# Optimization experiments

Hardware: AMD Instinct MI355X
Metric: run time of the kernel (lower is better)

## Reference

```python
import jax, jax.numpy as jnp
import numpy as np

E, TOPK, H, F, CAP, TP = 8, 2, 1024, 4096, 2048, 1
N = 8192  # tokens * topk (token copies)


def setup_inputs() -> dict:
    key = jax.random.key(0)
    ks = jax.random.split(key, 6)
    inputs_shard = jax.random.normal(ks[0], (N, H), jnp.float32)
    gate_weight = jax.random.uniform(ks[1], (N,), jnp.float32)
    choosed_experts = jax.random.randint(ks[2], (N,), 0, E, dtype=jnp.int32)
    new_index = jax.random.permutation(ks[3], N).astype(jnp.int32)
    w1 = jax.random.normal(ks[4], (E, F, H), jnp.float32) * 0.02
    w2 = jax.random.normal(ks[5], (E, H, F), jnp.float32) * 0.02
    return {"inputs_shard": inputs_shard, "gate_weight": gate_weight,
            "choosed_experts": choosed_experts, "new_index": new_index,
            "w1": w1, "w2": w2}


def _grouped_expert_mlp(x, experts, w1, w2):
    # capacity-based grouped GEMM: sort token copies by expert, pack into
    # (E, CAP, H), run batched fc1->gelu->fc2, unpack back to token order.
    n = x.shape[0]
    order = jnp.argsort(experts)                      # [N]
    se = experts[order]
    offsets = jnp.searchsorted(se, jnp.arange(E))     # start of each expert block
    rank = jnp.arange(n) - offsets[se]                # within-expert position
    valid = rank < CAP                                # CAP=2*N/E, ~never drops
    slot = jnp.where(valid, se * CAP + rank, E * CAP) # out-of-range -> dropped
    buf = jnp.zeros((E * CAP, x.shape[1]), x.dtype).at[slot].set(x[order], mode="drop")
    xe = buf.reshape(E, CAP, -1)                      # [E, CAP, H]
    h = jax.nn.gelu(jnp.einsum("ech,efh->ecf", xe, w1), approximate=False)
    ye = jnp.einsum("ecf,ehf->ech", h, w2).reshape(E * CAP, -1)
    y_sorted = jnp.where(valid[:, None], ye[jnp.clip(slot, 0, E * CAP - 1)], 0.0)
    return jnp.zeros_like(x).at[order].set(y_sorted)  # back to token-copy order


def reference(inputs_shard, gate_weight, choosed_experts, new_index, w1, w2):
    # expert compute, scaled by router probabilities (combine-side scaling)
    result = _grouped_expert_mlp(inputs_shard, choosed_experts, w1, w2)
    result = result * gate_weight[:, None]
    # scatter combine: output1[new_index] = result; full_output += output1
    full_output = jnp.zeros((N, H), result.dtype).at[new_index].set(result)
    # topk reduce: view(N//topk, topk, H).sum(1)
    topk_reduce = full_output.reshape(N // TOPK, TOPK, H).sum(1)
    # reduce_scatter over TP group; TP=1 => identity
    return topk_reduce
```

## Files before the change

### kernel.cpp

```cpp
#include <hip/hip_runtime.h>
#include <stdint.h>

#define N_TOK 8192
#define HDIM  1024
#define FDIM  4096
#define NEXP  8
#define MAXTILES 72

typedef __attribute__((ext_vector_type(8))) __bf16 bf16x8;
typedef __attribute__((ext_vector_type(8))) unsigned short ushort8v;
typedef __attribute__((ext_vector_type(4))) unsigned short ushort4v;
typedef __attribute__((ext_vector_type(4))) float floatx4;

__device__ __forceinline__ unsigned short f2bf(float f) {
  union { float f; uint32_t u; } v; v.f = f;
  uint32_t u = v.u;
  return (unsigned short)((u + 0x7FFFu + ((u >> 16) & 1u)) >> 16);
}

__device__ __forceinline__ void load_lds16(const void* g, void* l) {
  __builtin_amdgcn_global_load_lds(
      (const __attribute__((address_space(1))) void*)(uintptr_t)g,
      (__attribute__((address_space(3))) void*)(uint32_t)(uintptr_t)l,
      16, 0, 0);
}


__global__ void k_count(const int* __restrict__ experts, int* __restrict__ meta) {
  int i = blockIdx.x * 256 + threadIdx.x;
  atomicAdd(&meta[experts[i]], 1);
}

__global__ void k_plan(int* __restrict__ meta) {
  if (threadIdx.x == 0) {
    int off = 0, nt = 0;
    for (int e = 0; e < NEXP; ++e) {
      int c = meta[e];
      meta[8 + e] = off;
      meta[16 + e] = off;
      int t = (c + 127) >> 7;
      for (int k = 0; k < t; ++k) meta[32 + nt++] = (e << 16) | k;
      off += c;
    }
    meta[24] = nt;
  }
}

__global__ void k_scatter(const int* __restrict__ experts, int* __restrict__ meta,
                          int* __restrict__ order) {
  int i = blockIdx.x * 256 + threadIdx.x;
  int e = experts[i];
  int pos = atomicAdd(&meta[16 + e], 1);
  order[pos] = i;
}

__global__ void k_pack(const float* __restrict__ x, const int* __restrict__ order,
                       unsigned short* __restrict__ xs) {
  int s = blockIdx.x;
  int i = order[s];
  int t = threadIdx.x;
  float4 v = *(const float4*)(x + (size_t)i * HDIM + t * 4);
  ushort4v u;
  u[0] = f2bf(v.x); u[1] = f2bf(v.y); u[2] = f2bf(v.z); u[3] = f2bf(v.w);
  *(ushort4v*)(xs + (size_t)s * HDIM + t * 4) = u;
}

__global__ void k_cvt(const float* __restrict__ src, unsigned short* __restrict__ dst) {
  size_t i = ((size_t)blockIdx.x * 256 + threadIdx.x) * 4;
  float4 v = *(const float4*)(src + i);
  ushort4v u;
  u[0] = f2bf(v.x); u[1] = f2bf(v.y); u[2] = f2bf(v.z); u[3] = f2bf(v.w);
  *(ushort4v*)(dst + i) = u;
}

template <bool PRE>
__global__ __launch_bounds__(256) void gemm1_t(
    const unsigned short* __restrict__ xs, const void* __restrict__ w1v,
    unsigned short* __restrict__ h1, const int* __restrict__ meta) {
  __shared__ unsigned short As[128 * 32];
  __shared__ unsigned short Bs[128 * 32];

  int bx = blockIdx.z;
  if (bx >= meta[24]) return;
  int entry = meta[32 + bx];
  int e = entry >> 16, mt = entry & 0xffff;
  int row0 = meta[8 + e] + mt * 128;
  int rend = meta[8 + e] + meta[e];
  int fBase = blockIdx.x * 128;

  int tid = threadIdx.x;
  int w = tid >> 6, lane = tid & 63;
  int r = lane & 15, q = lane >> 4;
  int wm = (w >> 1) * 64, wn = (w & 1) * 64;

  int ar0 = (w * 16) + (lane >> 2);
  int s0 = min(row0 + ar0, N_TOK - 1);
  int s1 = min(row0 + 64 + ar0, N_TOK - 1);
  const unsigned short* ag0 = xs + (size_t)s0 * HDIM + (lane & 3) * 8;
  const unsigned short* ag1 = xs + (size_t)s1 * HDIM + (lane & 3) * 8;
  unsigned short* al0 = &As[(w * 16) * 32];
  unsigned short* al1 = &As[(64 + w * 16) * 32];

  const unsigned short* bg0 = nullptr; const unsigned short* bg1 = nullptr;
  unsigned short* bl0 = nullptr; unsigned short* bl1 = nullptr;
  const float* wbase = nullptr; int brow = 0, bkk = 0;
  if constexpr (PRE) {
    const unsigned short* wb = (const unsigned short*)w1v;
    int br = w * 16 + (lane >> 2);
    bg0 = wb + ((size_t)e * FDIM + fBase + br) * HDIM + (lane & 3) * 8;
    bg1 = bg0 + (size_t)64 * HDIM;
    bl0 = &Bs[(w * 16) * 32];
    bl1 = &Bs[(64 + w * 16) * 32];
  } else {
    brow = tid >> 1; bkk = (tid & 1) * 16;
    wbase = (const float*)w1v + ((size_t)e * FDIM + fBase + brow) * HDIM + bkk;
  }

  floatx4 acc[4][4];
#pragma unroll
  for (int i = 0; i < 4; ++i)
#pragma unroll
    for (int j = 0; j < 4; ++j) acc[i][j] = (floatx4){0.f, 0.f, 0.f, 0.f};

  for (int k0 = 0; k0 < HDIM; k0 += 32) {
    __syncthreads();
    load_lds16(ag0 + k0, al0);
    load_lds16(ag1 + k0, al1);
    if constexpr (PRE) {
      load_lds16(bg0 + k0, bl0);
      load_lds16(bg1 + k0, bl1);
    } else {
      const float* gb = wbase + k0;
      float4 f0 = *(const float4*)(gb);
      float4 f1 = *(const float4*)(gb + 4);
      float4 f2 = *(const float4*)(gb + 8);
      float4 f3 = *(const float4*)(gb + 12);
      ushort8v u0, u1;
      u0[0] = f2bf(f0.x); u0[1] = f2bf(f0.y); u0[2] = f2bf(f0.z); u0[3] = f2bf(f0.w);
      u0[4] = f2bf(f1.x); u0[5] = f2bf(f1.y); u0[6] = f2bf(f1.z); u0[7] = f2bf(f1.w);
      u1[0] = f2bf(f2.x); u1[1] = f2bf(f2.y); u1[2] = f2bf(f2.z); u1[3] = f2bf(f2.w);
      u1[4] = f2bf(f3.x); u1[5] = f2bf(f3.y); u1[6] = f2bf(f3.z); u1[7] = f2bf(f3.w);
      *(ushort8v*)&Bs[brow * 32 + bkk] = u0;
      *(ushort8v*)&Bs[brow * 32 + bkk + 8] = u1;
    }
    __syncthreads();

    bf16x8 av[4], bv[4];
#pragma unroll
    for (int i = 0; i < 4; ++i)
      av[i] = __builtin_bit_cast(bf16x8, *(const ushort8v*)&As[(wm + i * 16 + r) * 32 + q * 8]);
#pragma unroll
    for (int j = 0; j < 4; ++j)
      bv[j] = __builtin_bit_cast(bf16x8, *(const ushort8v*)&Bs[(wn + j * 16 + r) * 32 + q * 8]);
#pragma unroll
    for (int i = 0; i < 4; ++i)
#pragma unroll
      for (int j = 0; j < 4; ++j)
        acc[i][j] = __builtin_amdgcn_mfma_f32_16x16x32_bf16(av[i], bv[j], acc[i][j], 0, 0, 0);
  }

#pragma unroll
  for (int i = 0; i < 4; ++i) {
    int mrow = row0 + wm + i * 16 + q * 4;
#pragma unroll
    for (int reg = 0; reg < 4; ++reg) {
      int s = mrow + reg;
      if (s < rend) {
        unsigned short* dst = h1 + (size_t)s * FDIM + fBase + wn + r;
#pragma unroll
        for (int j = 0; j < 4; ++j) {
          float v = acc[i][j][reg];
          float g = 0.5f * v * (1.0f + erff(v * 0.70710678118654752f));
          dst[j * 16] = f2bf(g);
        }
      }
    }
  }
}

template <bool PRE>
__global__ __launch_bounds__(256) void gemm2_t(
    const unsigned short* __restrict__ h1, const void* __restrict__ w2v,
    const float* __restrict__ gate, const int* __restrict__ new_index,
    float* __restrict__ out, const int* __restrict__ meta) {
  __shared__ unsigned short As[128 * 32];
  __shared__ unsigned short Bs[128 * 32];

  int bx = blockIdx.z;
  if (bx >= meta[24]) return;
  int entry = meta[32 + bx];
  int e = entry >> 16, mt = entry & 0xffff;
  int row0 = meta[8 + e] + mt * 128;
  int rend = meta[8 + e] + meta[e];
  int nBase = blockIdx.x * 128;
  int kStart = blockIdx.y * (FDIM / 2);
  int kEnd = kStart + (FDIM / 2);
  const int* order = meta + 256;

  int tid = threadIdx.x;
  int w = tid >> 6, lane = tid & 63;
  int r = lane & 15, q = lane >> 4;
  int wm = (w >> 1) * 64, wn = (w & 1) * 64;

  int ar0 = (w * 16) + (lane >> 2);
  int s0 = min(row0 + ar0, N_TOK - 1);
  int s1 = min(row0 + 64 + ar0, N_TOK - 1);
  const unsigned short* ag0 = h1 + (size_t)s0 * FDIM + (lane & 3) * 8;
  const unsigned short* ag1 = h1 + (size_t)s1 * FDIM + (lane & 3) * 8;
  unsigned short* al0 = &As[(w * 16) * 32];
  unsigned short* al1 = &As[(64 + w * 16) * 32];

  const unsigned short* bg0 = nullptr; const unsigned short* bg1 = nullptr;
  unsigned short* bl0 = nullptr; unsigned short* bl1 = nullptr;
  const float* wbase = nullptr; int brow = 0, bkk = 0;
  if constexpr (PRE) {
    const unsigned short* wb = (const unsigned short*)w2v;
    int br = w * 16 + (lane >> 2);
    bg0 = wb + ((size_t)e * HDIM + nBase + br) * FDIM + (lane & 3) * 8;
    bg1 = bg0 + (size_t)64 * FDIM;
    bl0 = &Bs[(w * 16) * 32];
    bl1 = &Bs[(64 + w * 16) * 32];
  } else {
    brow = tid >> 1; bkk = (tid & 1) * 16;
    wbase = (const float*)w2v + ((size_t)e * HDIM + nBase + brow) * FDIM + bkk;
  }

  floatx4 acc[4][4];
#pragma unroll
  for (int i = 0; i < 4; ++i)
#pragma unroll
    for (int j = 0; j < 4; ++j) acc[i][j] = (floatx4){0.f, 0.f, 0.f, 0.f};

  for (int k0 = kStart; k0 < kEnd; k0 += 32) {
    __syncthreads();
    load_lds16(ag0 + k0, al0);
    load_lds16(ag1 + k0, al1);
    if constexpr (PRE) {
      load_lds16(bg0 + k0, bl0);
      load_lds16(bg1 + k0, bl1);
    } else {
      const float* gb = wbase + k0;
      float4 f0 = *(const float4*)(gb);
      float4 f1 = *(const float4*)(gb + 4);
      float4 f2 = *(const float4*)(gb + 8);
      float4 f3 = *(const float4*)(gb + 12);
      ushort8v u0, u1;
      u0[0] = f2bf(f0.x); u0[1] = f2bf(f0.y); u0[2] = f2bf(f0.z); u0[3] = f2bf(f0.w);
      u0[4] = f2bf(f1.x); u0[5] = f2bf(f1.y); u0[6] = f2bf(f1.z); u0[7] = f2bf(f1.w);
      u1[0] = f2bf(f2.x); u1[1] = f2bf(f2.y); u1[2] = f2bf(f2.z); u1[3] = f2bf(f2.w);
      u1[4] = f2bf(f3.x); u1[5] = f2bf(f3.y); u1[6] = f2bf(f3.z); u1[7] = f2bf(f3.w);
      *(ushort8v*)&Bs[brow * 32 + bkk] = u0;
      *(ushort8v*)&Bs[brow * 32 + bkk + 8] = u1;
    }
    __syncthreads();

    bf16x8 av[4], bv[4];
#pragma unroll
    for (int i = 0; i < 4; ++i)
      av[i] = __builtin_bit_cast(bf16x8, *(const ushort8v*)&As[(wm + i * 16 + r) * 32 + q * 8]);
#pragma unroll
    for (int j = 0; j < 4; ++j)
      bv[j] = __builtin_bit_cast(bf16x8, *(const ushort8v*)&Bs[(wn + j * 16 + r) * 32 + q * 8]);
#pragma unroll
    for (int i = 0; i < 4; ++i)
#pragma unroll
      for (int j = 0; j < 4; ++j)
        acc[i][j] = __builtin_amdgcn_mfma_f32_16x16x32_bf16(av[i], bv[j], acc[i][j], 0, 0, 0);
  }

#pragma unroll
  for (int i = 0; i < 4; ++i) {
    int mrow = row0 + wm + i * 16 + q * 4;
#pragma unroll
    for (int reg = 0; reg < 4; ++reg) {
      int s = mrow + reg;
      if (s < rend) {
        int itok = order[s];
        float gw = gate[itok];
        int jdx = new_index[itok];
        float* dst = out + (size_t)(jdx >> 1) * HDIM + nBase + wn + r;
#pragma unroll
        for (int j = 0; j < 4; ++j) atomicAdd(dst + j * 16, acc[i][j][reg] * gw);
      }
    }
  }
}

extern "C" void kernel_launch(void* const* d_in, const int* in_sizes, int n_in,
                              void* d_out, int out_size, void* d_ws, size_t ws_size,
                              hipStream_t stream) {
  const float* x        = (const float*)d_in[0];
  const float* gate     = (const float*)d_in[1];
  const int* experts    = (const int*)d_in[2];
  const int* new_index  = (const int*)d_in[3];
  const float* w1       = (const float*)d_in[4];
  const float* w2       = (const float*)d_in[5];
  float* out            = (float*)d_out;

  int* meta = (int*)d_ws;
  int* order = meta + 256;
  const size_t XS_OFF = 65536;
  const size_t XS_SZ  = (size_t)N_TOK * HDIM * 2;
  const size_t H1_SZ  = (size_t)N_TOK * FDIM * 2;
  const size_t W_SZ   = (size_t)NEXP * FDIM * HDIM * 2;
  unsigned short* xs  = (unsigned short*)((char*)d_ws + XS_OFF);
  unsigned short* h1  = (unsigned short*)((char*)d_ws + XS_OFF + XS_SZ);
  unsigned short* w1b = (unsigned short*)((char*)d_ws + XS_OFF + XS_SZ + H1_SZ);
  unsigned short* w2b = (unsigned short*)((char*)d_ws + XS_OFF + XS_SZ + H1_SZ + W_SZ);
  size_t need_small = XS_OFF + XS_SZ + H1_SZ;
  size_t need_big   = need_small + 2 * W_SZ;
  if (ws_size < need_small) return;
  bool big = ws_size >= need_big;

  hipMemsetAsync(d_ws, 0, 4096, stream);
  hipMemsetAsync(d_out, 0, (size_t)out_size * sizeof(float), stream);
  k_count<<<N_TOK / 256, 256, 0, stream>>>(experts, meta);
  k_plan<<<1, 64, 0, stream>>>(meta);
  k_scatter<<<N_TOK / 256, 256, 0, stream>>>(experts, meta, order);
  k_pack<<<N_TOK, 256, 0, stream>>>(x, order, xs);

  if (big) {
    int nblk = (int)((size_t)NEXP * FDIM * HDIM / 4 / 256);
    k_cvt<<<nblk, 256, 0, stream>>>(w1, w1b);
    k_cvt<<<nblk, 256, 0, stream>>>(w2, w2b);
    gemm1_t<true><<<dim3(FDIM / 128, 1, MAXTILES), 256, 0, stream>>>(xs, w1b, h1, meta);
    gemm2_t<true><<<dim3(HDIM / 128, 2, MAXTILES), 256, 0, stream>>>(h1, w2b, gate, new_index, out, meta);
  } else {
    gemm1_t<false><<<dim3(FDIM / 128, 1, MAXTILES), 256, 0, stream>>>(xs, w1, h1, meta);
    gemm2_t<false><<<dim3(HDIM / 128, 2, MAXTILES), 256, 0, stream>>>(h1, w2, gate, new_index, out, meta);
  }
}
```

Measured before the change: 674.7 us.

## Fuse weight conversion into pack/GEMM1 launches and double-buffer LDS in GEMMs

Merges the expert scatter with token packing and runs the w1 fp32-to-bf16 conversion in extra blocks of that same launch. The w2 conversion moves into extra z-blocks of the GEMM1 launch, so it can overlap with GEMM1 compute. Both GEMMs now double-buffer their LDS tiles, issuing the next K-slice load before computing the current one, which cuts one barrier per iteration. This doubles LDS use per block, which may lower occupancy, and the per-token atomic now runs in one thread per block.

```diff
diff --git a/kernel.cpp b/kernel.cpp
--- a/kernel.cpp
+++ b/kernel.cpp
@@ -6,6 +6,8 @@
 #define FDIM  4096
 #define NEXP  8
 #define MAXTILES 72
+#define CVTZ  8
+#define CVT1B 2048
 
 typedef __attribute__((ext_vector_type(8))) __bf16 bf16x8;
 typedef __attribute__((ext_vector_type(8))) unsigned short ushort8v;
@@ -46,41 +48,64 @@
   }
 }
 
-__global__ void k_scatter(const int* __restrict__ experts, int* __restrict__ meta,
-                          int* __restrict__ order) {
-  int i = blockIdx.x * 256 + threadIdx.x;
-  int e = experts[i];
-  int pos = atomicAdd(&meta[16 + e], 1);
-  order[pos] = i;
-}
-
-__global__ void k_pack(const float* __restrict__ x, const int* __restrict__ order,
-                       unsigned short* __restrict__ xs) {
-  int s = blockIdx.x;
-  int i = order[s];
+__global__ void k_scatterpack(const float* __restrict__ x, const int* __restrict__ experts,
+                              int* __restrict__ meta, int* __restrict__ order,
+                              unsigned short* __restrict__ xs,
+                              const float* __restrict__ w1, unsigned short* __restrict__ w1b) {
+  int b = blockIdx.x;
   int t = threadIdx.x;
-  float4 v = *(const float4*)(x + (size_t)i * HDIM + t * 4);
-  ushort4v u;
-  u[0] = f2bf(v.x); u[1] = f2bf(v.y); u[2] = f2bf(v.z); u[3] = f2bf(v.w);
-  *(ushort4v*)(xs + (size_t)s * HDIM + t * 4) = u;
-}
-
-__global__ void k_cvt(const float* __restrict__ src, unsigned short* __restrict__ dst) {
-  size_t i = ((size_t)blockIdx.x * 256 + threadIdx.x) * 4;
-  float4 v = *(const float4*)(src + i);
-  ushort4v u;
-  u[0] = f2bf(v.x); u[1] = f2bf(v.y); u[2] = f2bf(v.z); u[3] = f2bf(v.w);
-  *(ushort4v*)(dst + i) = u;
+  if (b < N_TOK) {
+    __shared__ int spos;
+    if (t == 0) {
+      int e = experts[b];
+      int pos = atomicAdd(&meta[16 + e], 1);
+      order[pos] = b;
+      spos = pos;
+    }
+    __syncthreads();
+    int s = spos;
+    float4 v = *(const float4*)(x + (size_t)b * HDIM + t * 4);
+    ushort4v u;
+    u[0] = f2bf(v.x); u[1] = f2bf(v.y); u[2] = f2bf(v.z); u[3] = f2bf(v.w);
+    *(ushort4v*)(xs + (size_t)s * HDIM + t * 4) = u;
+  } else {
+    int cb = b - N_TOK;
+    const int per = (int)((size_t)NEXP * FDIM * HDIM / 4 / CVT1B);
+    size_t base = (size_t)cb * per;
+    for (int j = t; j < per; j += 256) {
+      size_t idx = (base + j) * 4;
+      float4 v = *(const float4*)(w1 + idx);
+      ushort4v u;
+      u[0] = f2bf(v.x); u[1] = f2bf(v.y); u[2] = f2bf(v.z); u[3] = f2bf(v.w);
+      *(ushort4v*)(w1b + idx) = u;
+    }
+  }
 }
 
 template <bool PRE>
 __global__ __launch_bounds__(256) void gemm1_t(
     const unsigned short* __restrict__ xs, const void* __restrict__ w1v,
-    unsigned short* __restrict__ h1, const int* __restrict__ meta) {
-  __shared__ unsigned short As[128 * 32];
-  __shared__ unsigned short Bs[128 * 32];
-
-  int bx = blockIdx.z;
+    unsigned short* __restrict__ h1, const int* __restrict__ meta,
+    const float* __restrict__ w2src, unsigned short* __restrict__ w2dst) {
+  if constexpr (PRE) {
+    if (blockIdx.z < CVTZ) {
+      int cvtid = blockIdx.z * gridDim.x + blockIdx.x;
+      const int per = (int)((size_t)NEXP * HDIM * FDIM / 4 / (CVTZ * (FDIM / 128)));
+      size_t base = (size_t)cvtid * per;
+      for (int j = threadIdx.x; j < per; j += 256) {
+        size_t idx = (base + j) * 4;
+        float4 v = *(const float4*)(w2src + idx);
+        ushort4v u;
+        u[0] = f2bf(v.x); u[1] = f2bf(v.y); u[2] = f2bf(v.z); u[3] = f2bf(v.w);
+        *(ushort4v*)(w2dst + idx) = u;
+      }
+      return;
+    }
+  }
+  __shared__ unsigned short As[2 * 128 * 32];
+  __shared__ unsigned short Bs[2 * 128 * 32];
+
+  int bx = blockIdx.z - (PRE ? CVTZ : 0);
   if (bx >= meta[24]) return;
   int entry = meta[32 + bx];
   int e = entry >> 16, mt = entry & 0xffff;
@@ -116,21 +141,14 @@
     wbase = (const float*)w1v + ((size_t)e * FDIM + fBase + brow) * HDIM + bkk;
   }
 
-  floatx4 acc[4][4];
-#pragma unroll
-  for (int i = 0; i < 4; ++i)
-#pragma unroll
-    for (int j = 0; j < 4; ++j) acc[i][j] = (floatx4){0.f, 0.f, 0.f, 0.f};
-
-  for (int k0 = 0; k0 < HDIM; k0 += 32) {
-    __syncthreads();
-    load_lds16(ag0 + k0, al0);
-    load_lds16(ag1 + k0, al1);
+  auto stage = [&](int kk, int bo) {
+    load_lds16(ag0 + kk, al0 + bo);
+    load_lds16(ag1 + kk, al1 + bo);
     if constexpr (PRE) {
-      load_lds16(bg0 + k0, bl0);
-      load_lds16(bg1 + k0, bl1);
+      load_lds16(bg0 + kk, bl0 + bo);
+      load_lds16(bg1 + kk, bl1 + bo);
     } else {
-      const float* gb = wbase + k0;
+      const float* gb = wbase + kk;
       float4 f0 = *(const float4*)(gb);
       float4 f1 = *(const float4*)(gb + 4);
       float4 f2 = *(const float4*)(gb + 8);
@@ -140,18 +158,30 @@
       u0[4] = f2bf(f1.x); u0[5] = f2bf(f1.y); u0[6] = f2bf(f1.z); u0[7] = f2bf(f1.w);
       u1[0] = f2bf(f2.x); u1[1] = f2bf(f2.y); u1[2] = f2bf(f2.z); u1[3] = f2bf(f2.w);
       u1[4] = f2bf(f3.x); u1[5] = f2bf(f3.y); u1[6] = f2bf(f3.z); u1[7] = f2bf(f3.w);
-      *(ushort8v*)&Bs[brow * 32 + bkk] = u0;
-      *(ushort8v*)&Bs[brow * 32 + bkk + 8] = u1;
-    }
+      *(ushort8v*)&Bs[bo + brow * 32 + bkk] = u0;
+      *(ushort8v*)&Bs[bo + brow * 32 + bkk + 8] = u1;
+    }
+  };
+
+  floatx4 acc[4][4];
+#pragma unroll
+  for (int i = 0; i < 4; ++i)
+#pragma unroll
+    for (int j = 0; j < 4; ++j) acc[i][j] = (floatx4){0.f, 0.f, 0.f, 0.f};
+
+  stage(0, 0);
+  for (int k0 = 0; k0 < HDIM; k0 += 32) {
+    int bo = ((k0 >> 5) & 1) * 4096;
     __syncthreads();
+    if (k0 + 32 < HDIM) stage(k0 + 32, bo ^ 4096);
 
     bf16x8 av[4], bv[4];
 #pragma unroll
     for (int i = 0; i < 4; ++i)
-      av[i] = __builtin_bit_cast(bf16x8, *(const ushort8v*)&As[(wm + i * 16 + r) * 32 + q * 8]);
+      av[i] = __builtin_bit_cast(bf16x8, *(const ushort8v*)&As[bo + (wm + i * 16 + r) * 32 + q * 8]);
 #pragma unroll
     for (int j = 0; j < 4; ++j)
-      bv[j] = __builtin_bit_cast(bf16x8, *(const ushort8v*)&Bs[(wn + j * 16 + r) * 32 + q * 8]);
+      bv[j] = __builtin_bit_cast(bf16x8, *(const ushort8v*)&Bs[bo + (wn + j * 16 + r) * 32 + q * 8]);
 #pragma unroll
     for (int i = 0; i < 4; ++i)
 #pragma unroll
@@ -183,8 +213,8 @@
     const unsigned short* __restrict__ h1, const void* __restrict__ w2v,
     const float* __restrict__ gate, const int* __restrict__ new_index,
     float* __restrict__ out, const int* __restrict__ meta) {
-  __shared__ unsigned short As[128 * 32];
-  __shared__ unsigned short Bs[128 * 32];
+  __shared__ unsigned short As[2 * 128 * 32];
+  __shared__ unsigned short Bs[2 * 128 * 32];
 
   int bx = blockIdx.z;
   if (bx >= meta[24]) return;
@@ -225,21 +255,14 @@
     wbase = (const float*)w2v + ((size_t)e * HDIM + nBase + brow) * FDIM + bkk;
   }
 
-  floatx4 acc[4][4];
-#pragma unroll
-  for (int i = 0; i < 4; ++i)
-#pragma unroll
-    for (int j = 0; j < 4; ++j) acc[i][j] = (floatx4){0.f, 0.f, 0.f, 0.f};
-
-  for (int k0 = kStart; k0 < kEnd; k0 += 32) {
-    __syncthreads();
-    load_lds16(ag0 + k0, al0);
-    load_lds16(ag1 + k0, al1);
+  auto stage = [&](int kk, int bo) {
+    load_lds16(ag0 + kk, al0 + bo);
+    load_lds16(ag1 + kk, al1 + bo);
     if constexpr (PRE) {
-      load_lds16(bg0 + k0, bl0);
-      load_lds16(bg1 + k0, bl1);
+      load_lds16(bg0 + kk, bl0 + bo);
+      load_lds16(bg1 + kk, bl1 + bo);
     } else {
-      const float* gb = wbase + k0;
+      const float* gb = wbase + kk;
       float4 f0 = *(const float4*)(gb);
       float4 f1 = *(const float4*)(gb + 4);
       float4 f2 = *(const float4*)(gb + 8);
@@ -249,18 +272,30 @@
       u0[4] = f2bf(f1.x); u0[5] = f2bf(f1.y); u0[6] = f2bf(f1.z); u0[7] = f2bf(f1.w);
       u1[0] = f2bf(f2.x); u1[1] = f2bf(f2.y); u1[2] = f2bf(f2.z); u1[3] = f2bf(f2.w);
       u1[4] = f2bf(f3.x); u1[5] = f2bf(f3.y); u1[6] = f2bf(f3.z); u1[7] = f2bf(f3.w);
-      *(ushort8v*)&Bs[brow * 32 + bkk] = u0;
-      *(ushort8v*)&Bs[brow * 32 + bkk + 8] = u1;
-    }
+      *(ushort8v*)&Bs[bo + brow * 32 + bkk] = u0;
+      *(ushort8v*)&Bs[bo + brow * 32 + bkk + 8] = u1;
+    }
+  };
+
+  floatx4 acc[4][4];
+#pragma unroll
+  for (int i = 0; i < 4; ++i)
+#pragma unroll
+    for (int j = 0; j < 4; ++j) acc[i][j] = (floatx4){0.f, 0.f, 0.f, 0.f};
+
+  stage(kStart, 0);
+  for (int k0 = kStart; k0 < kEnd; k0 += 32) {
+    int bo = (((k0 - kStart) >> 5) & 1) * 4096;
     __syncthreads();
+    if (k0 + 32 < kEnd) stage(k0 + 32, bo ^ 4096);
 
     bf16x8 av[4], bv[4];
 #pragma unroll
     for (int i = 0; i < 4; ++i)
-      av[i] = __builtin_bit_cast(bf16x8, *(const ushort8v*)&As[(wm + i * 16 + r) * 32 + q * 8]);
+      av[i] = __builtin_bit_cast(bf16x8, *(const ushort8v*)&As[bo + (wm + i * 16 + r) * 32 + q * 8]);
 #pragma unroll
     for (int j = 0; j < 4; ++j)
-      bv[j] = __builtin_bit_cast(bf16x8, *(const ushort8v*)&Bs[(wn + j * 16 + r) * 32 + q * 8]);
+      bv[j] = __builtin_bit_cast(bf16x8, *(const ushort8v*)&Bs[bo + (wn + j * 16 + r) * 32 + q * 8]);
 #pragma unroll
     for (int i = 0; i < 4; ++i)
 #pragma unroll
@@ -316,17 +351,13 @@
   hipMemsetAsync(d_out, 0, (size_t)out_size * sizeof(float), stream);
   k_count<<<N_TOK / 256, 256, 0, stream>>>(experts, meta);
   k_plan<<<1, 64, 0, stream>>>(meta);
-  k_scatter<<<N_TOK / 256, 256, 0, stream>>>(experts, meta, order);
-  k_pack<<<N_TOK, 256, 0, stream>>>(x, order, xs);
+  k_scatterpack<<<N_TOK + (big ? CVT1B : 0), 256, 0, stream>>>(x, experts, meta, order, xs, w1, w1b);
 
   if (big) {
-    int nblk = (int)((size_t)NEXP * FDIM * HDIM / 4 / 256);
-    k_cvt<<<nblk, 256, 0, stream>>>(w1, w1b);
-    k_cvt<<<nblk, 256, 0, stream>>>(w2, w2b);
-    gemm1_t<true><<<dim3(FDIM / 128, 1, MAXTILES), 256, 0, stream>>>(xs, w1b, h1, meta);
+    gemm1_t<true><<<dim3(FDIM / 128, 1, MAXTILES + CVTZ), 256, 0, stream>>>(xs, w1b, h1, meta, w2, w2b);
     gemm2_t<true><<<dim3(HDIM / 128, 2, MAXTILES), 256, 0, stream>>>(h1, w2b, gate, new_index, out, meta);
   } else {
-    gemm1_t<false><<<dim3(FDIM / 128, 1, MAXTILES), 256, 0, stream>>>(xs, w1, h1, meta);
+    gemm1_t<false><<<dim3(FDIM / 128, 1, MAXTILES), 256, 0, stream>>>(xs, w1, h1, meta, nullptr, nullptr);
     gemm2_t<false><<<dim3(HDIM / 128, 2, MAXTILES), 256, 0, stream>>>(h1, w2, gate, new_index, out, meta);
   }
 }
```

After: 728.8 us. 8.0% more time.
